# Kernel optimization log

Measured on AMD Instinct MI355X. Metric: run time of the kernel, lower is better.

The kernel has to match this reference:

```python
import jax, jax.numpy as jnp
import numpy as np

B, C, L = 8, 256, 2048
D = C // 8  # q/k channel dim = 32


def setup_inputs() -> dict:
    key = jax.random.key(0)
    kx, kq, kk, kv, kg = jax.random.split(key, 5)
    kq1, kq2 = jax.random.split(kq)
    kk1, kk2 = jax.random.split(kk)
    kv1, kv2 = jax.random.split(kv)
    s = 0.05
    return {
        "x": jax.random.normal(kx, (B, C, L), dtype=jnp.float32),
        "Wq": jax.random.normal(kq1, (D, C), dtype=jnp.float32) * s,
        "bq": jax.random.normal(kq2, (D,), dtype=jnp.float32) * s,
        "Wk": jax.random.normal(kk1, (D, C), dtype=jnp.float32) * s,
        "bk": jax.random.normal(kk2, (D,), dtype=jnp.float32) * s,
        "Wv": jax.random.normal(kv1, (C, C), dtype=jnp.float32) * s,
        "bv": jax.random.normal(kv2, (C,), dtype=jnp.float32) * s,
        "gamma": jax.random.normal(kg, (1,), dtype=jnp.float32) * 0.1,
    }


def reference(x, Wq, bq, Wk, bk, Wv, bv, gamma):
    # 1x1 Conv1d == per-position channel matmul
    Q = jnp.einsum("dc,bcl->bld", Wq, x) + bq            # (B, L, D)
    K = jnp.einsum("dc,bcl->bdl", Wk, x) + bk[:, None]   # (B, D, L)
    V = jnp.einsum("oc,bcl->bol", Wv, x) + bv[:, None]   # (B, C, L)
    scale = jnp.float32(1.0 / np.sqrt(D))
    # attn[b, i, j]: softmax over j (keys)
    attn = jax.nn.softmax(jnp.einsum("bid,bdj->bij", Q, K) * scale, axis=-1)
    # out = V @ attn^T : out[b, c, i] = sum_j V[b, c, j] * attn[b, i, j]
    out = jnp.einsum("bcj,bij->bci", V, attn)            # (B, C, L)
    return gamma * out + x
```

## Files before the change

### kernel.cpp

```cpp
#include <hip/hip_runtime.h>
#include <stdint.h>


#define BB 8
#define CC 256
#define LL 2048
#define DD 32

typedef unsigned short u16;
typedef __attribute__((ext_vector_type(8))) short short8;
typedef __attribute__((ext_vector_type(4))) float f32x4;

#define SCALE_LOG2E 0.2550348612f

static __device__ __forceinline__ uint32_t pack2bf16(float hi, float lo) {
    return (__float_as_uint(hi) & 0xFFFF0000u) | (__float_as_uint(lo) >> 16);
}

static __device__ __forceinline__ float fexp2(float v) {
#if __has_builtin(__builtin_amdgcn_exp2f)
    return __builtin_amdgcn_exp2f(v);
#else
    return exp2f(v);
#endif
}

static __device__ __forceinline__ float frcp(float v) {
#if __has_builtin(__builtin_amdgcn_rcpf)
    return __builtin_amdgcn_rcpf(v);
#else
    return 1.0f / v;
#endif
}

__global__ __launch_bounds__(256) void prep_w_kernel(
    const float* __restrict__ Wq, const float* __restrict__ Wk,
    const float* __restrict__ Wv, u16* __restrict__ Wh)
{
    int idx = blockIdx.x * 256 + threadIdx.x;
    int r = idx >> 6;
    int c4 = (idx & 63) << 2;
    const float* src;
    if (r < 32)       src = Wq + (size_t)r * CC + c4;
    else if (r < 64)  src = Wk + (size_t)(r - 32) * CC + c4;
    else              src = Wv + (size_t)(r - 64) * CC + c4;
    float4 v = *(const float4*)src;
    uint2 o;
    o.x = pack2bf16(v.y, v.x);
    o.y = pack2bf16(v.w, v.z);
    *(uint2*)(Wh + (size_t)r * CC + c4) = o;
}

__global__ __launch_bounds__(512, 2) void proj_kernel(
    const float* __restrict__ x, const u16* __restrict__ Wh,
    const float* __restrict__ bq, const float* __restrict__ bk,
    const float* __restrict__ bv,
    u16* __restrict__ Qh, u16* __restrict__ Kth, u16* __restrict__ Vh)
{
    __shared__ u16 xls[32 * 264];
    const int blk = blockIdx.x;
    const int b = blk & 7;
    const int l0 = (blk >> 3) << 5;
    const int tid = threadIdx.x;
    const int w = tid >> 6;
    const int lane = tid & 63;
    const int ln = lane & 15;
    const int q = lane >> 4;

#pragma unroll
    for (int cc = 0; cc < 4; ++cc) {
        const int c = cc * 64 + (tid >> 3);
        const int l4 = (tid & 7) * 4;
        const float4 v = *(const float4*)(x + ((size_t)(b * CC + c)) * LL + l0 + l4);
        xls[(l4 + 0) * 264 + c] = (u16)(__float_as_uint(v.x) >> 16);
        xls[(l4 + 1) * 264 + c] = (u16)(__float_as_uint(v.y) >> 16);
        xls[(l4 + 2) * 264 + c] = (u16)(__float_as_uint(v.z) >> 16);
        xls[(l4 + 3) * 264 + c] = (u16)(__float_as_uint(v.w) >> 16);
    }
    __syncthreads();

    const int wl = w & 1;
    const int wm = w >> 1;
    const int mbase = wm * 80;
    const int l = l0 + wl * 16 + ln;

    f32x4 acc[5];
#pragma unroll
    for (int i = 0; i < 5; ++i) acc[i] = (f32x4){0.f, 0.f, 0.f, 0.f};

#pragma unroll
    for (int c0 = 0; c0 < CC; c0 += 32) {
        const short8 bf = *(const short8*)(&xls[(wl * 16 + ln) * 264 + c0 + q * 8]);
#pragma unroll
        for (int mt = 0; mt < 5; ++mt) {
            const short8 af = *(const short8*)(Wh + (size_t)(mbase + mt * 16 + ln) * CC + c0 + q * 8);
            acc[mt] = __builtin_amdgcn_mfma_f32_16x16x32_bf16(af, bf, acc[mt], 0, 0, 0);
        }
    }

#pragma unroll
    for (int mt = 0; mt < 5; ++mt) {
        const int rg = mbase + mt * 16 + q * 4;
        if (rg < 32) {
            float v0 = (acc[mt][0] + bq[rg + 0]) * SCALE_LOG2E;
            float v1 = (acc[mt][1] + bq[rg + 1]) * SCALE_LOG2E;
            float v2 = (acc[mt][2] + bq[rg + 2]) * SCALE_LOG2E;
            float v3 = (acc[mt][3] + bq[rg + 3]) * SCALE_LOG2E;
            uint2 o; o.x = pack2bf16(v1, v0); o.y = pack2bf16(v3, v2);
            *(uint2*)(Qh + ((size_t)(b * LL) + l) * DD + rg) = o;
        } else if (rg < 64) {
            const int rk = rg - 32;
            float v0 = acc[mt][0] + bk[rk + 0];
            float v1 = acc[mt][1] + bk[rk + 1];
            float v2 = acc[mt][2] + bk[rk + 2];
            float v3 = acc[mt][3] + bk[rk + 3];
            uint2 o; o.x = pack2bf16(v1, v0); o.y = pack2bf16(v3, v2);
            *(uint2*)(Kth + ((size_t)(b * LL) + l) * DD + rk) = o;
        } else {
            const int cv = rg - 64;
#pragma unroll
            for (int rr = 0; rr < 4; ++rr) {
                const float v = acc[mt][rr] + bv[cv + rr];
                Vh[((size_t)(b * CC) + cv + rr) * LL + l] = (u16)(__float_as_uint(v) >> 16);
            }
        }
    }
}

__global__ __launch_bounds__(512, 1) void attn_kernel(
    const u16* __restrict__ Qh, const u16* __restrict__ Kth,
    const u16* __restrict__ Vh, const float* __restrict__ x,
    const float* __restrict__ gamma, float* __restrict__ out)
{
    __shared__ u16 pbuf[8 * 64 * 40];
    __shared__ float obuf[256 * 68];
    __shared__ float lbuf[8 * 64];

    const int blk = blockIdx.x;
    const int b = blk & 7;
    const int i0 = (blk >> 3) << 6;
    const int tid = threadIdx.x;
    const int w = tid >> 6;
    const int wc = w >> 2;
    const int wj = w & 3;
    const int lane = tid & 63;
    const int ln = lane & 15;
    const int q = lane >> 4;

    u16* pb = pbuf + w * (64 * 40);
    const u16* Qb = Qh + ((size_t)(b * LL) + i0) * DD;
    const u16* Kb = Kth + (size_t)(b * LL) * DD;
    const u16* Vb = Vh + ((size_t)(b * CC) + wc * 128) * LL;

    short8 qf[4];
#pragma unroll
    for (int it = 0; it < 4; ++it)
        qf[it] = *(const short8*)(Qb + (size_t)(it * 16 + ln) * DD + q * 8);

    const f32x4 zf = {0.f, 0.f, 0.f, 0.f};
    f32x4 oacc[8][4];
#pragma unroll
    for (int a = 0; a < 8; ++a)
#pragma unroll
        for (int c = 0; c < 4; ++c) oacc[a][c] = zf;
    float lsum[4] = {0.f, 0.f, 0.f, 0.f};

    int jb = wj * 32;
    short8 kf0 = *(const short8*)(Kb + (size_t)(jb + ln) * DD + q * 8);
    short8 kf1 = *(const short8*)(Kb + (size_t)(jb + 16 + ln) * DD + q * 8);

    for (int n = 0; n < 16; ++n) {
        jb = n * 128 + wj * 32;
        const int jnx = (n < 15) ? (n + 1) * 128 + wj * 32 : jb;

        short8 vf[8];
#pragma unroll
        for (int ct = 0; ct < 8; ++ct)
            vf[ct] = *(const short8*)(Vb + (size_t)(ct * 16 + ln) * LL + jb + q * 8);
        const short8 kn0 = *(const short8*)(Kb + (size_t)(jnx + ln) * DD + q * 8);
        const short8 kn1 = *(const short8*)(Kb + (size_t)(jnx + 16 + ln) * DD + q * 8);

#pragma unroll
        for (int jt = 0; jt < 2; ++jt) {
            const short8 kf = jt ? kf1 : kf0;
#pragma unroll
            for (int it = 0; it < 4; ++it) {
                const f32x4 st = __builtin_amdgcn_mfma_f32_16x16x32_bf16(kf, qf[it], zf, 0, 0, 0);
                const float e0 = fexp2(st[0]), e1 = fexp2(st[1]);
                const float e2 = fexp2(st[2]), e3 = fexp2(st[3]);
                lsum[it] += (e0 + e1) + (e2 + e3);
                uint2 d; d.x = pack2bf16(e1, e0); d.y = pack2bf16(e3, e2);
                *(uint2*)(&pb[(it * 16 + ln) * 40 + jt * 16 + q * 4]) = d;
            }
        }

        short8 pf[4];
#pragma unroll
        for (int it = 0; it < 4; ++it)
            pf[it] = *(const short8*)(&pb[(it * 16 + ln) * 40 + q * 8]);

#pragma unroll
        for (int ct = 0; ct < 8; ++ct)
#pragma unroll
            for (int it = 0; it < 4; ++it)
                oacc[ct][it] = __builtin_amdgcn_mfma_f32_16x16x32_bf16(vf[ct], pf[it], oacc[ct][it], 0, 0, 0);

        kf0 = kn0; kf1 = kn1;
    }

#pragma unroll
    for (int it = 0; it < 4; ++it) {
        float s = lsum[it];
        s += __shfl_xor(s, 16);
        s += __shfl_xor(s, 32);
        lsum[it] = s;
    }
    if (q == 0) {
#pragma unroll
        for (int it = 0; it < 4; ++it) lbuf[w * 64 + it * 16 + ln] = lsum[it];
    }

#pragma unroll
    for (int p = 0; p < 4; ++p) {
        if (wj == p) {
#pragma unroll
            for (int ct = 0; ct < 8; ++ct)
#pragma unroll
                for (int it = 0; it < 4; ++it) {
                    const int i = it * 16 + ln;
#pragma unroll
                    for (int r = 0; r < 4; ++r) {
                        const int c = wc * 128 + ct * 16 + q * 4 + r;
                        if (p == 0) obuf[c * 68 + i] = oacc[ct][it][r];
                        else        obuf[c * 68 + i] += oacc[ct][it][r];
                    }
                }
        }
        __syncthreads();
    }

    const float g = gamma[0];
    const int i4 = (tid & 15) * 4;
    float4 sv = {0.f, 0.f, 0.f, 0.f};
#pragma unroll
    for (int ww = 0; ww < 8; ++ww) {
        const float4 lv = *(const float4*)&lbuf[ww * 64 + i4];
        sv.x += lv.x; sv.y += lv.y; sv.z += lv.z; sv.w += lv.w;
    }
    float4 li;
    li.x = 2.0f * frcp(sv.x); li.y = 2.0f * frcp(sv.y);
    li.z = 2.0f * frcp(sv.z); li.w = 2.0f * frcp(sv.w);

#pragma unroll
    for (int cc = 0; cc < 8; ++cc) {
        const int c = cc * 32 + (tid >> 4);
        const float4 ov = *(const float4*)&obuf[c * 68 + i4];
        const size_t idx = ((size_t)(b * CC + c)) * LL + i0 + i4;
        const float4 xv = *(const float4*)(x + idx);
        float4 o;
        o.x = g * (ov.x * li.x) + xv.x;
        o.y = g * (ov.y * li.y) + xv.y;
        o.z = g * (ov.z * li.z) + xv.z;
        o.w = g * (ov.w * li.w) + xv.w;
        *(float4*)(out + idx) = o;
    }
}

extern "C" void kernel_launch(void* const* d_in, const int* in_sizes, int n_in,
                              void* d_out, int out_size, void* d_ws, size_t ws_size,
                              hipStream_t stream)
{
    const float* x     = (const float*)d_in[0];
    const float* Wq    = (const float*)d_in[1];
    const float* bq    = (const float*)d_in[2];
    const float* Wk    = (const float*)d_in[3];
    const float* bk    = (const float*)d_in[4];
    const float* Wv    = (const float*)d_in[5];
    const float* bv    = (const float*)d_in[6];
    const float* gamma = (const float*)d_in[7];
    float* out = (float*)d_out;

    uint8_t* ws = (uint8_t*)d_ws;
    u16* Wh  = (u16*)(ws + 0x000000);
    u16* Qh  = (u16*)(ws + 0x040000);
    u16* Kth = (u16*)(ws + 0x140000);
    u16* Vh  = (u16*)(ws + 0x240000);

    prep_w_kernel<<<80, 256, 0, stream>>>(Wq, Wk, Wv, Wh);
    proj_kernel<<<512, 512, 0, stream>>>(x, Wh, bq, bk, bv, Qh, Kth, Vh);
    attn_kernel<<<256, 512, 0, stream>>>(Qh, Kth, Vh, x, gamma, out);
}
```

Measured before the change: 148.9 us.

## Fuse weight conversion into projection and split attention across 16 waves

Drops the separate weight-prep kernel. The projection kernel now converts fp32 weights to bf16 in LDS itself, working on 64-position tiles with 2 N-tiles per wave. The attention kernel moves to 1024 threads, with each wave covering 64 channels instead of 128. This halves per-wave accumulators and V fragments and reuses the P scratch space as the output reduction buffer. It removes one launch and aims for more waves to hide latency, at the cost of losing the K prefetch, adding an extra barrier, and re-converting weights in every projection block.

```diff
diff --git a/kernel.cpp b/kernel.cpp
--- a/kernel.cpp
+++ b/kernel.cpp
@@ -33,108 +33,124 @@
 #endif
 }
 
-__global__ __launch_bounds__(256) void prep_w_kernel(
-    const float* __restrict__ Wq, const float* __restrict__ Wk,
-    const float* __restrict__ Wv, u16* __restrict__ Wh)
-{
-    int idx = blockIdx.x * 256 + threadIdx.x;
-    int r = idx >> 6;
-    int c4 = (idx & 63) << 2;
-    const float* src;
-    if (r < 32)       src = Wq + (size_t)r * CC + c4;
-    else if (r < 64)  src = Wk + (size_t)(r - 32) * CC + c4;
-    else              src = Wv + (size_t)(r - 64) * CC + c4;
-    float4 v = *(const float4*)src;
-    uint2 o;
-    o.x = pack2bf16(v.y, v.x);
-    o.y = pack2bf16(v.w, v.z);
-    *(uint2*)(Wh + (size_t)r * CC + c4) = o;
-}
-
 __global__ __launch_bounds__(512, 2) void proj_kernel(
-    const float* __restrict__ x, const u16* __restrict__ Wh,
-    const float* __restrict__ bq, const float* __restrict__ bk,
-    const float* __restrict__ bv,
+    const float* __restrict__ x,
+    const float* __restrict__ Wq, const float* __restrict__ bq,
+    const float* __restrict__ Wk, const float* __restrict__ bk,
+    const float* __restrict__ Wv, const float* __restrict__ bv,
     u16* __restrict__ Qh, u16* __restrict__ Kth, u16* __restrict__ Vh)
 {
-    __shared__ u16 xls[32 * 264];
+    __shared__ u16 xls[64 * 264];
+    __shared__ u16 Wls[320 * 40];
     const int blk = blockIdx.x;
     const int b = blk & 7;
-    const int l0 = (blk >> 3) << 5;
+    const int l0 = (blk >> 3) << 6;
     const int tid = threadIdx.x;
     const int w = tid >> 6;
     const int lane = tid & 63;
     const int ln = lane & 15;
     const int q = lane >> 4;
-
-#pragma unroll
-    for (int cc = 0; cc < 4; ++cc) {
-        const int c = cc * 64 + (tid >> 3);
-        const int l4 = (tid & 7) * 4;
-        const float4 v = *(const float4*)(x + ((size_t)(b * CC + c)) * LL + l0 + l4);
-        xls[(l4 + 0) * 264 + c] = (u16)(__float_as_uint(v.x) >> 16);
-        xls[(l4 + 1) * 264 + c] = (u16)(__float_as_uint(v.y) >> 16);
-        xls[(l4 + 2) * 264 + c] = (u16)(__float_as_uint(v.z) >> 16);
-        xls[(l4 + 3) * 264 + c] = (u16)(__float_as_uint(v.w) >> 16);
-    }
-    __syncthreads();
-
-    const int wl = w & 1;
     const int wm = w >> 1;
-    const int mbase = wm * 80;
-    const int l = l0 + wl * 16 + ln;
-
-    f32x4 acc[5];
-#pragma unroll
-    for (int i = 0; i < 5; ++i) acc[i] = (f32x4){0.f, 0.f, 0.f, 0.f};
-
-#pragma unroll
-    for (int c0 = 0; c0 < CC; c0 += 32) {
-        const short8 bf = *(const short8*)(&xls[(wl * 16 + ln) * 264 + c0 + q * 8]);
+    const int wn = w & 1;
+
+#pragma unroll
+    for (int i = 0; i < 2; ++i) {
+        const int id = tid + i * 512;
+        const int r = (id >> 4) << 2;
+        const int l4 = (id & 15) << 2;
+        union { float4 v; float f[4]; } vv[4];
+#pragma unroll
+        for (int k = 0; k < 4; ++k)
+            vv[k].v = *(const float4*)(x + ((size_t)(b * CC + r + k)) * LL + l0 + l4);
+#pragma unroll
+        for (int k = 0; k < 4; ++k) {
+            uint2 d;
+            d.x = pack2bf16(vv[1].f[k], vv[0].f[k]);
+            d.y = pack2bf16(vv[3].f[k], vv[2].f[k]);
+            *(uint2*)(&xls[(l4 + k) * 264 + r]) = d;
+        }
+    }
+
+    f32x4 acc[5][2];
+#pragma unroll
+    for (int a = 0; a < 5; ++a)
+#pragma unroll
+        for (int c = 0; c < 2; ++c) acc[a][c] = (f32x4){0.f, 0.f, 0.f, 0.f};
+
+    for (int kk = 0; kk < 8; ++kk) {
+        const int k0 = kk * 32;
+        __syncthreads();
+#pragma unroll
+        for (int i = 0; i < 5; ++i) {
+            const int id = tid + i * 512;
+            const int r = id >> 3;
+            const int c4 = (id & 7) << 2;
+            const float* src = (r < 32) ? (Wq + (size_t)r * CC)
+                             : (r < 64) ? (Wk + (size_t)(r - 32) * CC)
+                                        : (Wv + (size_t)(r - 64) * CC);
+            union { float4 v; float f[4]; } t;
+            t.v = *(const float4*)(src + k0 + c4);
+            uint2 d;
+            d.x = pack2bf16(t.f[1], t.f[0]);
+            d.y = pack2bf16(t.f[3], t.f[2]);
+            *(uint2*)(&Wls[r * 40 + c4]) = d;
+        }
+        __syncthreads();
+
+        short8 bf[2];
+#pragma unroll
+        for (int nt = 0; nt < 2; ++nt)
+            bf[nt] = *(const short8*)(&xls[(wn * 32 + nt * 16 + ln) * 264 + k0 + q * 8]);
 #pragma unroll
         for (int mt = 0; mt < 5; ++mt) {
-            const short8 af = *(const short8*)(Wh + (size_t)(mbase + mt * 16 + ln) * CC + c0 + q * 8);
-            acc[mt] = __builtin_amdgcn_mfma_f32_16x16x32_bf16(af, bf, acc[mt], 0, 0, 0);
+            const short8 af = *(const short8*)(&Wls[(wm * 80 + mt * 16 + ln) * 40 + q * 8]);
+            acc[mt][0] = __builtin_amdgcn_mfma_f32_16x16x32_bf16(af, bf[0], acc[mt][0], 0, 0, 0);
+            acc[mt][1] = __builtin_amdgcn_mfma_f32_16x16x32_bf16(af, bf[1], acc[mt][1], 0, 0, 0);
         }
     }
 
 #pragma unroll
     for (int mt = 0; mt < 5; ++mt) {
-        const int rg = mbase + mt * 16 + q * 4;
-        if (rg < 32) {
-            float v0 = (acc[mt][0] + bq[rg + 0]) * SCALE_LOG2E;
-            float v1 = (acc[mt][1] + bq[rg + 1]) * SCALE_LOG2E;
-            float v2 = (acc[mt][2] + bq[rg + 2]) * SCALE_LOG2E;
-            float v3 = (acc[mt][3] + bq[rg + 3]) * SCALE_LOG2E;
-            uint2 o; o.x = pack2bf16(v1, v0); o.y = pack2bf16(v3, v2);
-            *(uint2*)(Qh + ((size_t)(b * LL) + l) * DD + rg) = o;
-        } else if (rg < 64) {
-            const int rk = rg - 32;
-            float v0 = acc[mt][0] + bk[rk + 0];
-            float v1 = acc[mt][1] + bk[rk + 1];
-            float v2 = acc[mt][2] + bk[rk + 2];
-            float v3 = acc[mt][3] + bk[rk + 3];
-            uint2 o; o.x = pack2bf16(v1, v0); o.y = pack2bf16(v3, v2);
-            *(uint2*)(Kth + ((size_t)(b * LL) + l) * DD + rk) = o;
-        } else {
-            const int cv = rg - 64;
-#pragma unroll
-            for (int rr = 0; rr < 4; ++rr) {
-                const float v = acc[mt][rr] + bv[cv + rr];
-                Vh[((size_t)(b * CC) + cv + rr) * LL + l] = (u16)(__float_as_uint(v) >> 16);
+        const int rg = wm * 80 + mt * 16 + q * 4;
+#pragma unroll
+        for (int nt = 0; nt < 2; ++nt) {
+            const int l = l0 + wn * 32 + nt * 16 + ln;
+            if (rg < 32) {
+                float v0 = (acc[mt][nt][0] + bq[rg + 0]) * SCALE_LOG2E;
+                float v1 = (acc[mt][nt][1] + bq[rg + 1]) * SCALE_LOG2E;
+                float v2 = (acc[mt][nt][2] + bq[rg + 2]) * SCALE_LOG2E;
+                float v3 = (acc[mt][nt][3] + bq[rg + 3]) * SCALE_LOG2E;
+                uint2 o; o.x = pack2bf16(v1, v0); o.y = pack2bf16(v3, v2);
+                *(uint2*)(Qh + ((size_t)(b * LL) + l) * DD + rg) = o;
+            } else if (rg < 64) {
+                const int rk = rg - 32;
+                float v0 = acc[mt][nt][0] + bk[rk + 0];
+                float v1 = acc[mt][nt][1] + bk[rk + 1];
+                float v2 = acc[mt][nt][2] + bk[rk + 2];
+                float v3 = acc[mt][nt][3] + bk[rk + 3];
+                uint2 o; o.x = pack2bf16(v1, v0); o.y = pack2bf16(v3, v2);
+                *(uint2*)(Kth + ((size_t)(b * LL) + l) * DD + rk) = o;
+            } else {
+                const int cv = rg - 64;
+#pragma unroll
+                for (int rr = 0; rr < 4; ++rr) {
+                    const float v = acc[mt][nt][rr] + bv[cv + rr];
+                    Vh[((size_t)(b * CC) + cv + rr) * LL + l] = (u16)(__float_as_uint(v) >> 16);
+                }
             }
         }
     }
 }
 
-__global__ __launch_bounds__(512, 1) void attn_kernel(
+__global__ __launch_bounds__(1024, 4) void attn_kernel(
     const u16* __restrict__ Qh, const u16* __restrict__ Kth,
     const u16* __restrict__ Vh, const float* __restrict__ x,
     const float* __restrict__ gamma, float* __restrict__ out)
 {
-    __shared__ u16 pbuf[8 * 64 * 40];
-    __shared__ float obuf[256 * 68];
-    __shared__ float lbuf[8 * 64];
+    __shared__ __align__(16) char smem[81920];
+    __shared__ float lbuf[16 * 64];
+    u16* pbuf = (u16*)smem;
+    float* obuf = (float*)smem;
 
     const int blk = blockIdx.x;
     const int b = blk & 7;
@@ -150,7 +166,7 @@
     u16* pb = pbuf + w * (64 * 40);
     const u16* Qb = Qh + ((size_t)(b * LL) + i0) * DD;
     const u16* Kb = Kth + (size_t)(b * LL) * DD;
-    const u16* Vb = Vh + ((size_t)(b * CC) + wc * 128) * LL;
+    const u16* Vb = Vh + ((size_t)(b * CC) + wc * 64) * LL;
 
     short8 qf[4];
 #pragma unroll
@@ -158,27 +174,22 @@
         qf[it] = *(const short8*)(Qb + (size_t)(it * 16 + ln) * DD + q * 8);
 
     const f32x4 zf = {0.f, 0.f, 0.f, 0.f};
-    f32x4 oacc[8][4];
-#pragma unroll
-    for (int a = 0; a < 8; ++a)
+    f32x4 oacc[4][4];
+#pragma unroll
+    for (int a = 0; a < 4; ++a)
 #pragma unroll
         for (int c = 0; c < 4; ++c) oacc[a][c] = zf;
     float lsum[4] = {0.f, 0.f, 0.f, 0.f};
 
-    int jb = wj * 32;
-    short8 kf0 = *(const short8*)(Kb + (size_t)(jb + ln) * DD + q * 8);
-    short8 kf1 = *(const short8*)(Kb + (size_t)(jb + 16 + ln) * DD + q * 8);
-
     for (int n = 0; n < 16; ++n) {
-        jb = n * 128 + wj * 32;
-        const int jnx = (n < 15) ? (n + 1) * 128 + wj * 32 : jb;
-
-        short8 vf[8];
-#pragma unroll
-        for (int ct = 0; ct < 8; ++ct)
+        const int jb = n * 128 + wj * 32;
+
+        const short8 kf0 = *(const short8*)(Kb + (size_t)(jb + ln) * DD + q * 8);
+        const short8 kf1 = *(const short8*)(Kb + (size_t)(jb + 16 + ln) * DD + q * 8);
+        short8 vf[4];
+#pragma unroll
+        for (int ct = 0; ct < 4; ++ct)
             vf[ct] = *(const short8*)(Vb + (size_t)(ct * 16 + ln) * LL + jb + q * 8);
-        const short8 kn0 = *(const short8*)(Kb + (size_t)(jnx + ln) * DD + q * 8);
-        const short8 kn1 = *(const short8*)(Kb + (size_t)(jnx + 16 + ln) * DD + q * 8);
 
 #pragma unroll
         for (int jt = 0; jt < 2; ++jt) {
@@ -194,18 +205,13 @@
             }
         }
 
-        short8 pf[4];
-#pragma unroll
-        for (int it = 0; it < 4; ++it)
-            pf[it] = *(const short8*)(&pb[(it * 16 + ln) * 40 + q * 8]);
-
-#pragma unroll
-        for (int ct = 0; ct < 8; ++ct)
-#pragma unroll
-            for (int it = 0; it < 4; ++it)
-                oacc[ct][it] = __builtin_amdgcn_mfma_f32_16x16x32_bf16(vf[ct], pf[it], oacc[ct][it], 0, 0, 0);
-
-        kf0 = kn0; kf1 = kn1;
+#pragma unroll
+        for (int it = 0; it < 4; ++it) {
+            const short8 pf = *(const short8*)(&pb[(it * 16 + ln) * 40 + q * 8]);
+#pragma unroll
+            for (int ct = 0; ct < 4; ++ct)
+                oacc[ct][it] = __builtin_amdgcn_mfma_f32_16x16x32_bf16(vf[ct], pf, oacc[ct][it], 0, 0, 0);
+        }
     }
 
 #pragma unroll
@@ -219,18 +225,19 @@
 #pragma unroll
         for (int it = 0; it < 4; ++it) lbuf[w * 64 + it * 16 + ln] = lsum[it];
     }
+    __syncthreads();
 
 #pragma unroll
     for (int p = 0; p < 4; ++p) {
         if (wj == p) {
 #pragma unroll
-            for (int ct = 0; ct < 8; ++ct)
+            for (int ct = 0; ct < 4; ++ct)
 #pragma unroll
                 for (int it = 0; it < 4; ++it) {
                     const int i = it * 16 + ln;
 #pragma unroll
                     for (int r = 0; r < 4; ++r) {
-                        const int c = wc * 128 + ct * 16 + q * 4 + r;
+                        const int c = wc * 64 + ct * 16 + q * 4 + r;
                         if (p == 0) obuf[c * 68 + i] = oacc[ct][it][r];
                         else        obuf[c * 68 + i] += oacc[ct][it][r];
                     }
@@ -243,17 +250,17 @@
     const int i4 = (tid & 15) * 4;
     float4 sv = {0.f, 0.f, 0.f, 0.f};
 #pragma unroll
-    for (int ww = 0; ww < 8; ++ww) {
+    for (int ww = 0; ww < 16; ++ww) {
         const float4 lv = *(const float4*)&lbuf[ww * 64 + i4];
         sv.x += lv.x; sv.y += lv.y; sv.z += lv.z; sv.w += lv.w;
     }
     float4 li;
-    li.x = 2.0f * frcp(sv.x); li.y = 2.0f * frcp(sv.y);
-    li.z = 2.0f * frcp(sv.z); li.w = 2.0f * frcp(sv.w);
-
-#pragma unroll
-    for (int cc = 0; cc < 8; ++cc) {
-        const int c = cc * 32 + (tid >> 4);
+    li.x = 4.0f * frcp(sv.x); li.y = 4.0f * frcp(sv.y);
+    li.z = 4.0f * frcp(sv.z); li.w = 4.0f * frcp(sv.w);
+
+#pragma unroll
+    for (int cc = 0; cc < 4; ++cc) {
+        const int c = cc * 64 + (tid >> 4);
         const float4 ov = *(const float4*)&obuf[c * 68 + i4];
         const size_t idx = ((size_t)(b * CC + c)) * LL + i0 + i4;
         const float4 xv = *(const float4*)(x + idx);
@@ -281,12 +288,10 @@
     float* out = (float*)d_out;
 
     uint8_t* ws = (uint8_t*)d_ws;
-    u16* Wh  = (u16*)(ws + 0x000000);
-    u16* Qh  = (u16*)(ws + 0x040000);
-    u16* Kth = (u16*)(ws + 0x140000);
-    u16* Vh  = (u16*)(ws + 0x240000);
-
-    prep_w_kernel<<<80, 256, 0, stream>>>(Wq, Wk, Wv, Wh);
-    proj_kernel<<<512, 512, 0, stream>>>(x, Wh, bq, bk, bv, Qh, Kth, Vh);
-    attn_kernel<<<256, 512, 0, stream>>>(Qh, Kth, Vh, x, gamma, out);
-}
+    u16* Qh  = (u16*)(ws + 0x000000);
+    u16* Kth = (u16*)(ws + 0x100000);
+    u16* Vh  = (u16*)(ws + 0x200000);
+
+    proj_kernel<<<256, 512, 0, stream>>>(x, Wq, bq, Wk, bk, Wv, bv, Qh, Kth, Vh);
+    attn_kernel<<<256, 1024, 0, stream>>>(Qh, Kth, Vh, x, gamma, out);
+}
```

After: 221.2 us. 1.49x slower.

## Software-pipeline score/exp stage with double-buffered P and share LDS with output buffer

Applied to the files above, without the earlier changes.

The attention loop now computes the exp'd scores for the next key block into a second P buffer while the current block's PV MFMAs run, so exp and LDS writes overlap with matrix work. The P buffers and the output reduction buffer are aliased in one shared allocation, with an added barrier, which cuts LDS use so two blocks can fit per CU (launch bounds raised to 2). The projection kernel packs four channels per bf16 store when transposing x into LDS instead of doing scalar 16-bit stores, and its occupancy hint goes up to 4. Workspace offsets are also reordered. Higher occupancy limits may force register spills given the large oacc array.

```diff
diff --git a/kernel.cpp b/kernel.cpp
--- a/kernel.cpp
+++ b/kernel.cpp
@@ -51,7 +51,7 @@
     *(uint2*)(Wh + (size_t)r * CC + c4) = o;
 }
 
-__global__ __launch_bounds__(512, 2) void proj_kernel(
+__global__ __launch_bounds__(512, 4) void proj_kernel(
     const float* __restrict__ x, const u16* __restrict__ Wh,
     const float* __restrict__ bq, const float* __restrict__ bk,
     const float* __restrict__ bv,
@@ -66,41 +66,45 @@
     const int lane = tid & 63;
     const int ln = lane & 15;
     const int q = lane >> 4;
-
-#pragma unroll
-    for (int cc = 0; cc < 4; ++cc) {
-        const int c = cc * 64 + (tid >> 3);
-        const int l4 = (tid & 7) * 4;
-        const float4 v = *(const float4*)(x + ((size_t)(b * CC + c)) * LL + l0 + l4);
-        xls[(l4 + 0) * 264 + c] = (u16)(__float_as_uint(v.x) >> 16);
-        xls[(l4 + 1) * 264 + c] = (u16)(__float_as_uint(v.y) >> 16);
-        xls[(l4 + 2) * 264 + c] = (u16)(__float_as_uint(v.z) >> 16);
-        xls[(l4 + 3) * 264 + c] = (u16)(__float_as_uint(v.w) >> 16);
+    const int wm = w >> 1;
+    const int wn = w & 1;
+
+    {
+        const int r = (tid >> 3) << 2;
+        const int l4 = (tid & 7) << 2;
+        union { float4 v; float f[4]; } vv[4];
+#pragma unroll
+        for (int k = 0; k < 4; ++k)
+            vv[k].v = *(const float4*)(x + ((size_t)(b * CC + r + k)) * LL + l0 + l4);
+#pragma unroll
+        for (int k = 0; k < 4; ++k) {
+            uint2 d;
+            d.x = pack2bf16(vv[1].f[k], vv[0].f[k]);
+            d.y = pack2bf16(vv[3].f[k], vv[2].f[k]);
+            *(uint2*)(&xls[(l4 + k) * 264 + r]) = d;
+        }
     }
     __syncthreads();
 
-    const int wl = w & 1;
-    const int wm = w >> 1;
-    const int mbase = wm * 80;
-    const int l = l0 + wl * 16 + ln;
-
     f32x4 acc[5];
 #pragma unroll
-    for (int i = 0; i < 5; ++i) acc[i] = (f32x4){0.f, 0.f, 0.f, 0.f};
-
-#pragma unroll
-    for (int c0 = 0; c0 < CC; c0 += 32) {
-        const short8 bf = *(const short8*)(&xls[(wl * 16 + ln) * 264 + c0 + q * 8]);
+    for (int a = 0; a < 5; ++a) acc[a] = (f32x4){0.f, 0.f, 0.f, 0.f};
+
+#pragma unroll
+    for (int kk = 0; kk < 8; ++kk) {
+        const int k0 = kk * 32;
+        const short8 bf = *(const short8*)(&xls[(wn * 16 + ln) * 264 + k0 + q * 8]);
 #pragma unroll
         for (int mt = 0; mt < 5; ++mt) {
-            const short8 af = *(const short8*)(Wh + (size_t)(mbase + mt * 16 + ln) * CC + c0 + q * 8);
+            const short8 af = *(const short8*)(Wh + (size_t)(wm * 80 + mt * 16 + ln) * CC + k0 + q * 8);
             acc[mt] = __builtin_amdgcn_mfma_f32_16x16x32_bf16(af, bf, acc[mt], 0, 0, 0);
         }
     }
 
+    const int l = l0 + wn * 16 + ln;
 #pragma unroll
     for (int mt = 0; mt < 5; ++mt) {
-        const int rg = mbase + mt * 16 + q * 4;
+        const int rg = wm * 80 + mt * 16 + q * 4;
         if (rg < 32) {
             float v0 = (acc[mt][0] + bq[rg + 0]) * SCALE_LOG2E;
             float v1 = (acc[mt][1] + bq[rg + 1]) * SCALE_LOG2E;
@@ -127,14 +131,15 @@
     }
 }
 
-__global__ __launch_bounds__(512, 1) void attn_kernel(
+__global__ __launch_bounds__(512, 2) void attn_kernel(
     const u16* __restrict__ Qh, const u16* __restrict__ Kth,
     const u16* __restrict__ Vh, const float* __restrict__ x,
     const float* __restrict__ gamma, float* __restrict__ out)
 {
-    __shared__ u16 pbuf[8 * 64 * 40];
-    __shared__ float obuf[256 * 68];
+    __shared__ __align__(16) char smem[81920];
     __shared__ float lbuf[8 * 64];
+    u16* pbuf = (u16*)smem;
+    float* obuf = (float*)smem;
 
     const int blk = blockIdx.x;
     const int b = blk & 7;
@@ -147,7 +152,8 @@
     const int ln = lane & 15;
     const int q = lane >> 4;
 
-    u16* pb = pbuf + w * (64 * 40);
+    u16* pb0 = pbuf + w * (64 * 40);
+    u16* pb1 = pbuf + (8 + w) * (64 * 40);
     const u16* Qb = Qh + ((size_t)(b * LL) + i0) * DD;
     const u16* Kb = Kth + (size_t)(b * LL) * DD;
     const u16* Vb = Vh + ((size_t)(b * CC) + wc * 128) * LL;
@@ -165,24 +171,13 @@
         for (int c = 0; c < 4; ++c) oacc[a][c] = zf;
     float lsum[4] = {0.f, 0.f, 0.f, 0.f};
 
-    int jb = wj * 32;
-    short8 kf0 = *(const short8*)(Kb + (size_t)(jb + ln) * DD + q * 8);
-    short8 kf1 = *(const short8*)(Kb + (size_t)(jb + 16 + ln) * DD + q * 8);
-
-    for (int n = 0; n < 16; ++n) {
-        jb = n * 128 + wj * 32;
-        const int jnx = (n < 15) ? (n + 1) * 128 + wj * 32 : jb;
-
-        short8 vf[8];
-#pragma unroll
-        for (int ct = 0; ct < 8; ++ct)
-            vf[ct] = *(const short8*)(Vb + (size_t)(ct * 16 + ln) * LL + jb + q * 8);
-        const short8 kn0 = *(const short8*)(Kb + (size_t)(jnx + ln) * DD + q * 8);
-        const short8 kn1 = *(const short8*)(Kb + (size_t)(jnx + 16 + ln) * DD + q * 8);
-
+    {
+        const int jb = wj * 32;
+        const short8 k0f = *(const short8*)(Kb + (size_t)(jb + ln) * DD + q * 8);
+        const short8 k1f = *(const short8*)(Kb + (size_t)(jb + 16 + ln) * DD + q * 8);
 #pragma unroll
         for (int jt = 0; jt < 2; ++jt) {
-            const short8 kf = jt ? kf1 : kf0;
+            const short8 kf = jt ? k1f : k0f;
 #pragma unroll
             for (int it = 0; it < 4; ++it) {
                 const f32x4 st = __builtin_amdgcn_mfma_f32_16x16x32_bf16(kf, qf[it], zf, 0, 0, 0);
@@ -190,14 +185,47 @@
                 const float e2 = fexp2(st[2]), e3 = fexp2(st[3]);
                 lsum[it] += (e0 + e1) + (e2 + e3);
                 uint2 d; d.x = pack2bf16(e1, e0); d.y = pack2bf16(e3, e2);
-                *(uint2*)(&pb[(it * 16 + ln) * 40 + jt * 16 + q * 4]) = d;
+                *(uint2*)(&pb0[(it * 16 + ln) * 40 + jt * 16 + q * 4]) = d;
             }
         }
+    }
+    short8 sk0 = *(const short8*)(Kb + (size_t)(128 + wj * 32 + ln) * DD + q * 8);
+    short8 sk1 = *(const short8*)(Kb + (size_t)(128 + wj * 32 + 16 + ln) * DD + q * 8);
+
+    for (int n = 0; n < 16; ++n) {
+        u16* pbc = (n & 1) ? pb1 : pb0;
+        u16* pbn = (n & 1) ? pb0 : pb1;
+        const int jb = n * 128 + wj * 32;
 
         short8 pf[4];
 #pragma unroll
         for (int it = 0; it < 4; ++it)
-            pf[it] = *(const short8*)(&pb[(it * 16 + ln) * 40 + q * 8]);
+            pf[it] = *(const short8*)(&pbc[(it * 16 + ln) * 40 + q * 8]);
+
+        short8 vf[8];
+#pragma unroll
+        for (int ct = 0; ct < 8; ++ct)
+            vf[ct] = *(const short8*)(Vb + (size_t)(ct * 16 + ln) * LL + jb + q * 8);
+
+        const int jn2 = (n + 2 < 16) ? (n + 2) * 128 + wj * 32 : jb;
+        const short8 nk0 = *(const short8*)(Kb + (size_t)(jn2 + ln) * DD + q * 8);
+        const short8 nk1 = *(const short8*)(Kb + (size_t)(jn2 + 16 + ln) * DD + q * 8);
+
+        if (n < 15) {
+#pragma unroll
+            for (int jt = 0; jt < 2; ++jt) {
+                const short8 kf = jt ? sk1 : sk0;
+#pragma unroll
+                for (int it = 0; it < 4; ++it) {
+                    const f32x4 st = __builtin_amdgcn_mfma_f32_16x16x32_bf16(kf, qf[it], zf, 0, 0, 0);
+                    const float e0 = fexp2(st[0]), e1 = fexp2(st[1]);
+                    const float e2 = fexp2(st[2]), e3 = fexp2(st[3]);
+                    lsum[it] += (e0 + e1) + (e2 + e3);
+                    uint2 d; d.x = pack2bf16(e1, e0); d.y = pack2bf16(e3, e2);
+                    *(uint2*)(&pbn[(it * 16 + ln) * 40 + jt * 16 + q * 4]) = d;
+                }
+            }
+        }
 
 #pragma unroll
         for (int ct = 0; ct < 8; ++ct)
@@ -205,7 +233,7 @@
             for (int it = 0; it < 4; ++it)
                 oacc[ct][it] = __builtin_amdgcn_mfma_f32_16x16x32_bf16(vf[ct], pf[it], oacc[ct][it], 0, 0, 0);
 
-        kf0 = kn0; kf1 = kn1;
+        sk0 = nk0; sk1 = nk1;
     }
 
 #pragma unroll
@@ -219,6 +247,7 @@
 #pragma unroll
         for (int it = 0; it < 4; ++it) lbuf[w * 64 + it * 16 + ln] = lsum[it];
     }
+    __syncthreads();
 
 #pragma unroll
     for (int p = 0; p < 4; ++p) {
@@ -281,10 +310,10 @@
     float* out = (float*)d_out;
 
     uint8_t* ws = (uint8_t*)d_ws;
-    u16* Wh  = (u16*)(ws + 0x000000);
-    u16* Qh  = (u16*)(ws + 0x040000);
-    u16* Kth = (u16*)(ws + 0x140000);
-    u16* Vh  = (u16*)(ws + 0x240000);
+    u16* Qh  = (u16*)(ws + 0x000000);
+    u16* Kth = (u16*)(ws + 0x100000);
+    u16* Vh  = (u16*)(ws + 0x200000);
+    u16* Wh  = (u16*)(ws + 0xA00000);
 
     prep_w_kernel<<<80, 256, 0, stream>>>(Wq, Wk, Wv, Wh);
     proj_kernel<<<512, 512, 0, stream>>>(x, Wh, bq, bk, bv, Qh, Kth, Vh);
```

After: 149.3 us. About the same (+0.3%).
